# Kernel tuning notes

Measured on AMD Instinct MI355X. Metric: run time of the kernel, lower is better.

Reference implementation:

```python
import jax, jax.numpy as jnp
import numpy as np

B, S, H, NH = 4, 2048, 1024, 16
HS = H // NH  # head size 64


def setup_inputs() -> dict:
    key = jax.random.key(0)
    ks = jax.random.split(key, 12)
    inv = 1.0 / np.sqrt(H)
    d = {
        "query": jax.random.normal(ks[0], (B, S, H), jnp.float32),
        "key": jax.random.normal(ks[1], (B, S, H), jnp.float32),
        "value": jax.random.normal(ks[2], (B, S, H), jnp.float32),
        "causal_mask": jnp.tril(jnp.ones((S, S), dtype=bool)),
        "Wq": jax.random.uniform(ks[3], (H, H), jnp.float32, -inv, inv),
        "bq": jax.random.uniform(ks[4], (H,), jnp.float32, -inv, inv),
        "Wk": jax.random.uniform(ks[5], (H, H), jnp.float32, -inv, inv),
        "bk": jax.random.uniform(ks[6], (H,), jnp.float32, -inv, inv),
        "Wv": jax.random.uniform(ks[7], (H, H), jnp.float32, -inv, inv),
        "bv": jax.random.uniform(ks[8], (H,), jnp.float32, -inv, inv),
        "Wo": jax.random.uniform(ks[9], (H, H), jnp.float32, -inv, inv),
        "bo": jax.random.uniform(ks[10], (H,), jnp.float32, -inv, inv),
    }
    return d


def reference(query, key, value, causal_mask, Wq, bq, Wk, bk, Wv, bv, Wo, bo):
    # Linear projections (torch Linear: x @ W.T + b)
    q = query @ Wq.T + bq
    k = key @ Wk.T + bk
    v = value @ Wv.T + bv
    # [B, NH, S, HS]
    q = q.reshape(B, S, NH, HS).transpose(0, 2, 1, 3)
    k = k.reshape(B, S, NH, HS).transpose(0, 2, 1, 3)
    v = v.reshape(B, S, NH, HS).transpose(0, 2, 1, 3)
    scores = jnp.einsum("bhqd,bhkd->bhqk", q, k) / jnp.sqrt(jnp.float32(HS))
    scores = jnp.where(causal_mask[None, None, :, :], scores, -jnp.inf)
    attn = jax.nn.softmax(scores, axis=-1)
    ctx = jnp.einsum("bhqk,bhkd->bhqd", attn, v)
    ctx = ctx.transpose(0, 2, 1, 3).reshape(B, S, H)
    return ctx @ Wo.T + bo
```

## Files before the change

kernel.cpp:

```cpp
#include <hip/hip_runtime.h>
#include <hip/hip_bf16.h>
#include <math.h>

#define B_  4
#define S_  2048
#define H_  1024
#define NH_ 16
#define HS_ 64

typedef __attribute__((ext_vector_type(8))) short bf16x8;
typedef __attribute__((ext_vector_type(4))) short bf16x4;
typedef __attribute__((ext_vector_type(4))) float f32x4;

#define QSCALE_ (0.125f * 1.44269504f)

__device__ __forceinline__ short f2bf(float f) {
    unsigned u = __builtin_bit_cast(unsigned, f);
    u += 0x7FFFu + ((u >> 16) & 1u);
    return (short)(u >> 16);
}

typedef __attribute__((address_space(3))) void lds_void;
typedef const __attribute__((address_space(1))) void g_void;
__device__ __forceinline__ void gl_lds16(const void* g, void* l) {
    __builtin_amdgcn_global_load_lds((g_void*)g, (lds_void*)l, 16, 0, 0);
}


__global__ __launch_bounds__(256) void cvt_all_k(
    const float* __restrict__ a0, const float* __restrict__ a1,
    const float* __restrict__ a2, const float* __restrict__ w0,
    const float* __restrict__ w1, const float* __restrict__ w2,
    const float* __restrict__ w3,
    short* o0, short* o1, short* o2, short* o3, short* o4, short* o5, short* o6)
{
    const int y = blockIdx.y;
    const float* ins[7]  = {a0, a1, a2, w0, w1, w2, w3};
    short*       outs[7] = {o0, o1, o2, o3, o4, o5, o6};
    const int n8 = (y < 3) ? (int)((size_t)B_ * S_ * H_ / 8) : (int)((size_t)H_ * H_ / 8);
    const int i = blockIdx.x * 256 + threadIdx.x;
    if (i >= n8) return;
    const float4* p = (const float4*)ins[y] + (size_t)i * 2;
    float4 a = p[0], b = p[1];
    bf16x8 o;
    o[0] = f2bf(a.x); o[1] = f2bf(a.y); o[2] = f2bf(a.z); o[3] = f2bf(a.w);
    o[4] = f2bf(b.x); o[5] = f2bf(b.y); o[6] = f2bf(b.z); o[7] = f2bf(b.w);
    *(bf16x8*)(outs[y] + (size_t)i * 8) = o;
}

__device__ __forceinline__ void gemm_core(
    const short* __restrict__ A, const short* __restrict__ W,
    int m0, int n0, short* As, short* Ws, f32x4 acc[4][4])
{
    const int tid  = threadIdx.x;
    const int w    = tid >> 6;
    const int lane = tid & 63;
    const int l15  = lane & 15;
    const int q4   = lane >> 4;
    const int wm   = w >> 1;
    const int wn   = w & 1;
    const int K    = 1024;
    const int swz  = l15 & 7;

    const char* Abase = (const char*)A + (size_t)m0 * K * 2;
    const char* Wbase = (const char*)W + (size_t)n0 * K * 2;

    #pragma unroll
    for (int mi = 0; mi < 4; ++mi)
        #pragma unroll
        for (int ni = 0; ni < 4; ++ni)
            acc[mi][ni] = (f32x4){0.f, 0.f, 0.f, 0.f};

    for (int k0 = 0; k0 < K; k0 += 64) {
        __syncthreads();
        #pragma unroll
        for (int t = 0; t < 4; ++t) {
            const int ob  = t * 4096 + w * 1024;
            const int idx = t * 256 + w * 64 + lane;
            const int row = idx >> 3;
            const int sc  = (idx & 7) ^ (row & 7);
            gl_lds16(Abase + (size_t)row * (K * 2) + k0 * 2 + sc * 16, (char*)As + ob);
            gl_lds16(Wbase + (size_t)row * (K * 2) + k0 * 2 + sc * 16, (char*)Ws + ob);
        }
        __syncthreads();

        #pragma unroll
        for (int kh = 0; kh < 2; ++kh) {
            bf16x8 af[4], bf[4];
            #pragma unroll
            for (int mi = 0; mi < 4; ++mi)
                af[mi] = *(const bf16x8*)(As + (wm * 64 + mi * 16 + l15) * 64
                                             + (((kh * 4 + q4) ^ swz) * 8));
            #pragma unroll
            for (int ni = 0; ni < 4; ++ni)
                bf[ni] = *(const bf16x8*)(Ws + (wn * 64 + ni * 16 + l15) * 64
                                             + (((kh * 4 + q4) ^ swz) * 8));
            #pragma unroll
            for (int mi = 0; mi < 4; ++mi)
                #pragma unroll
                for (int ni = 0; ni < 4; ++ni)
                    acc[mi][ni] = __builtin_amdgcn_mfma_f32_16x16x32_bf16(
                        af[mi], bf[ni], acc[mi][ni], 0, 0, 0);
        }
    }
}

__global__ __launch_bounds__(256) void gemm_proj_k(
    const short* __restrict__ Aq, const short* __restrict__ Wqb,
    const float* __restrict__ bq, short* __restrict__ qb,
    const short* __restrict__ Ak, const short* __restrict__ Wkb,
    const float* __restrict__ bk, short* __restrict__ kb,
    const short* __restrict__ Wvb, const short* __restrict__ Av,
    const float* __restrict__ bv, short* __restrict__ vtb)
{
    __shared__ short As[128 * 64];
    __shared__ short Ws[128 * 64];

    const int z = blockIdx.z;
    const short *A, *W; const float* bias; short* out;
    if (z == 0)      { A = Aq;  W = Wqb; bias = bq; out = qb;  }
    else if (z == 1) { A = Ak;  W = Wkb; bias = bk; out = kb;  }
    else             { A = Wvb; W = Av;  bias = bv; out = vtb; }
    const int m0 = (z == 2 ? blockIdx.y : blockIdx.x) * 128;
    const int n0 = (z == 2 ? blockIdx.x : blockIdx.y) * 128;

    f32x4 acc[4][4];
    gemm_core(A, W, m0, n0, As, Ws, acc);

    const int tid  = threadIdx.x;
    const int w    = tid >> 6;
    const int lane = tid & 63;
    const int l15  = lane & 15;
    const int q4   = lane >> 4;
    const int wm   = w >> 1;
    const int wn   = w & 1;

    #pragma unroll
    for (int mi = 0; mi < 4; ++mi) {
        #pragma unroll
        for (int r = 0; r < 4; ++r) {
            const int m = m0 + wm * 64 + mi * 16 + q4 * 4 + r;
            #pragma unroll
            for (int ni = 0; ni < 4; ++ni) {
                const int n = n0 + wn * 64 + ni * 16 + l15;
                float v = acc[mi][ni][r] + bias[z == 2 ? m : n];
                if (z == 0) v *= QSCALE_;
                if (z != 2) {
                    const int b = m >> 11, s = m & (S_ - 1);
                    const int h = n >> 6,  d = n & (HS_ - 1);
                    out[(((size_t)b * NH_ + h) * S_ + s) * HS_ + d] = f2bf(v);
                } else {
                    const int b = n >> 11, s = n & (S_ - 1);
                    const int h = m >> 6,  d = m & (HS_ - 1);
                    out[(((size_t)b * NH_ + h) * HS_ + d) * S_ + s] = f2bf(v);
                }
            }
        }
    }
}

__global__ __launch_bounds__(256) void gemm_out_k(
    const short* __restrict__ A, const short* __restrict__ W,
    const float* __restrict__ bias, float* __restrict__ Cout)
{
    __shared__ short As[128 * 64];
    __shared__ short Ws[128 * 64];
    const int m0 = blockIdx.x * 128;
    const int n0 = blockIdx.y * 128;

    f32x4 acc[4][4];
    gemm_core(A, W, m0, n0, As, Ws, acc);

    const int tid  = threadIdx.x;
    const int w    = tid >> 6;
    const int lane = tid & 63;
    const int l15  = lane & 15;
    const int q4   = lane >> 4;
    const int wm   = w >> 1;
    const int wn   = w & 1;

    #pragma unroll
    for (int mi = 0; mi < 4; ++mi)
        #pragma unroll
        for (int r = 0; r < 4; ++r) {
            const int m = m0 + wm * 64 + mi * 16 + q4 * 4 + r;
            #pragma unroll
            for (int ni = 0; ni < 4; ++ni) {
                const int n = n0 + wn * 64 + ni * 16 + l15;
                Cout[(size_t)m * H_ + n] = acc[mi][ni][r] + bias[n];
            }
        }
}

#define PPAD_ 72

__global__ __launch_bounds__(256) void attn_mfma(
    const short* __restrict__ Q, const short* __restrict__ K,
    const short* __restrict__ VT, short* __restrict__ O)
{
    __shared__ short Ks[2][64 * 64];
    __shared__ short Vt[2][64 * 64];
    __shared__ short Pl[4][32 * PPAD_];

    const int tid  = threadIdx.x;
    const int w    = tid >> 6;
    const int lane = tid & 63;
    const int l15  = lane & 15;
    const int q4   = lane >> 4;
    const int swz  = l15 & 7;

    const int old = blockIdx.x;
    const int rid = (old & 7) * 128 + (old >> 3);
    const int bh  = rid >> 4;
    const int qt  = 15 - (rid & 15);

    const size_t base = (size_t)bh * S_ * HS_;
    const int b = bh >> 4;
    const int h = bh & 15;

#define STAGE_KV(slot_, kt_)                                                      \
    do {                                                                          \
        _Pragma("unroll")                                                         \
        for (int t = 0; t < 2; ++t) {                                             \
            const int ob  = (slot_) * 8192 + t * 4096 + w * 1024;                 \
            const int idx = t * 256 + w * 64 + lane;        \
            const int r   = idx >> 3;                                             \
            const int sc  = (idx & 7) ^ (r & 7);          \
            gl_lds16(K + base + (size_t)((kt_) * 64 + r) * HS_ + sc * 8,          \
                     (char*)Ks + ob);                                             \
            gl_lds16(VT + base + (size_t)r * S_ + (kt_) * 64 + sc * 8,            \
                     (char*)Vt + ob);                                             \
        }                                                                         \
    } while (0)

    const int ktmax = 2 * qt + 1;

    STAGE_KV(0, 0);

    bf16x8 aQ[2][2];
    #pragma unroll
    for (int mi = 0; mi < 2; ++mi) {
        const int qrow = qt * 128 + w * 32 + mi * 16 + l15;
        #pragma unroll
        for (int kh = 0; kh < 2; ++kh)
            aQ[mi][kh] = *(const bf16x8*)(Q + base + (size_t)qrow * HS_ + kh * 32 + q4 * 8);
    }

    f32x4 accO[2][4];
    float lsum[2];
    #pragma unroll
    for (int mi = 0; mi < 2; ++mi) {
        #pragma unroll
        for (int db = 0; db < 4; ++db) accO[mi][db] = (f32x4){0.f, 0.f, 0.f, 0.f};
        lsum[mi] = 0.f;
    }

    __syncthreads();

    for (int kt = 0; kt <= ktmax; ++kt) {
        const int cur = kt & 1;
        if (kt < ktmax) STAGE_KV(cur ^ 1, kt + 1);

        f32x4 sbT[2][4];
        const short* KsBase = &Ks[cur][0];
        __builtin_amdgcn_s_setprio(1);
        #pragma unroll
        for (int nb = 0; nb < 4; ++nb) {
            const short* krow = KsBase + (nb * 16 + l15) * 64;
            bf16x8 k0 = *(const bf16x8*)(krow + ((q4 ^ swz) * 8));
            bf16x8 k1 = *(const bf16x8*)(krow + (((4 + q4) ^ swz) * 8));
            #pragma unroll
            for (int mi = 0; mi < 2; ++mi) {
                f32x4 a = (f32x4){0.f, 0.f, 0.f, 0.f};
                a = __builtin_amdgcn_mfma_f32_16x16x32_bf16(k0, aQ[mi][0], a, 0, 0, 0);
                a = __builtin_amdgcn_mfma_f32_16x16x32_bf16(k1, aQ[mi][1], a, 0, 0, 0);
                sbT[mi][nb] = a;
            }
        }
        __builtin_amdgcn_s_setprio(0);

        const bool need_mask = (kt >= 2 * qt);
        #pragma unroll
        for (int mi = 0; mi < 2; ++mi) {
            const int qrow = qt * 128 + w * 32 + mi * 16 + l15;
            #pragma unroll
            for (int nb = 0; nb < 4; ++nb) {
                float pr[4];
                #pragma unroll
                for (int r = 0; r < 4; ++r) {
                    float sv = sbT[mi][nb][r];
                    if (need_mask) {
                        const int kj = kt * 64 + nb * 16 + q4 * 4 + r;
                        if (kj > qrow) sv = -INFINITY;
                    }
                    const float p = exp2f(sv);
                    lsum[mi] += p;
                    pr[r] = p;
                }
                unsigned plo, phi;
                asm("v_cvt_pk_bf16_f32 %0, %1, %2" : "=v"(plo) : "v"(pr[0]), "v"(pr[1]));
                asm("v_cvt_pk_bf16_f32 %0, %1, %2" : "=v"(phi) : "v"(pr[2]), "v"(pr[3]));
                uint2 pk; pk.x = plo; pk.y = phi;
                *(uint2*)&Pl[w][(mi * 16 + l15) * PPAD_ + nb * 16 + q4 * 4] = pk;
            }
        }

        bf16x8 aP[2][2];
        #pragma unroll
        for (int mi = 0; mi < 2; ++mi)
            #pragma unroll
            for (int kh = 0; kh < 2; ++kh)
                aP[mi][kh] = *(const bf16x8*)(&Pl[w][(mi * 16 + l15) * PPAD_ + kh * 32 + q4 * 8]);
        const short* VtBase = &Vt[cur][0];
        __builtin_amdgcn_s_setprio(1);
        #pragma unroll
        for (int db = 0; db < 4; ++db) {
            const short* vrow = VtBase + (db * 16 + l15) * 64;
            bf16x8 v0 = *(const bf16x8*)(vrow + ((q4 ^ swz) * 8));
            bf16x8 v1 = *(const bf16x8*)(vrow + (((4 + q4) ^ swz) * 8));
            #pragma unroll
            for (int mi = 0; mi < 2; ++mi) {
                accO[mi][db] = __builtin_amdgcn_mfma_f32_16x16x32_bf16(aP[mi][0], v0, accO[mi][db], 0, 0, 0);
                accO[mi][db] = __builtin_amdgcn_mfma_f32_16x16x32_bf16(aP[mi][1], v1, accO[mi][db], 0, 0, 0);
            }
        }
        __builtin_amdgcn_s_setprio(0);

        __syncthreads();
    }

    #pragma unroll
    for (int mi = 0; mi < 2; ++mi) {
        float ls = lsum[mi];
        ls += __shfl_xor(ls, 16);
        ls += __shfl_xor(ls, 32);
        #pragma unroll
        for (int r = 0; r < 4; ++r) {
            const float inv = 1.f / __shfl(ls, q4 * 4 + r);
            const int orow = qt * 128 + w * 32 + mi * 16 + q4 * 4 + r;
            short* op = O + ((size_t)(b * S_ + orow)) * H_ + h * HS_;
            #pragma unroll
            for (int db = 0; db < 4; ++db)
                op[db * 16 + l15] = f2bf(accO[mi][db][r] * inv);
        }
    }
#undef STAGE_KV
}

extern "C" void kernel_launch(void* const* d_in, const int* in_sizes, int n_in,
                              void* d_out, int out_size, void* d_ws, size_t ws_size,
                              hipStream_t stream)
{
    const float* query = (const float*)d_in[0];
    const float* key   = (const float*)d_in[1];
    const float* value = (const float*)d_in[2];
    const float* Wq = (const float*)d_in[4];
    const float* bq = (const float*)d_in[5];
    const float* Wk = (const float*)d_in[6];
    const float* bk = (const float*)d_in[7];
    const float* Wv = (const float*)d_in[8];
    const float* bv = (const float*)d_in[9];
    const float* Wo = (const float*)d_in[10];
    const float* bo = (const float*)d_in[11];
    float* out = (float*)d_out;

    const size_t EA = (size_t)B_ * S_ * H_;
    const size_t EW = (size_t)H_ * H_;

    short* Aq  = (short*)d_ws;
    short* Ak  = Aq  + EA;
    short* Av  = Ak  + EA;
    short* Wqb = Av  + EA;
    short* Wkb = Wqb + EW;
    short* Wvb = Wkb + EW;
    short* Wob = Wvb + EW;
    short* qb  = Wob + EW;
    short* kb  = qb  + EA;
    short* vtb = kb  + EA;
    short* cb  = vtb + EA;

    const int M = B_ * S_;

    cvt_all_k<<<dim3((int)(EA / 8 / 256), 7), 256, 0, stream>>>(
        query, key, value, Wq, Wk, Wv, Wo,
        Aq, Ak, Av, Wqb, Wkb, Wvb, Wob);

    gemm_proj_k<<<dim3(M / 128, H_ / 128, 3), 256, 0, stream>>>(
        Aq, Wqb, bq, qb, Ak, Wkb, bk, kb, Wvb, Av, bv, vtb);

    attn_mfma<<<dim3(1024), 256, 0, stream>>>(qb, kb, vtb, cb);

    gemm_out_k<<<dim3(M / 128, H_ / 128), 256, 0, stream>>>(cb, Wob, bo, out);
}
```

Baseline: 394.5 us.

## Drop LDS staging in attention; load K/V fragments directly per wave

Rewrites the attention kernel so each wave loads its K and V^T MFMA fragments straight from global memory in 32-key blocks, with no shared-memory double buffering and no __syncthreads. The P tile now stays in registers: the packed bf16 exponentials are fed straight into the PV MFMA instead of going through an LDS round trip. Each wave also runs its own causal trip count (qs), and block-to-XCD mapping uses a new interleaved q-tile order for load balance. This removes LDS traffic and block-wide barriers but relies on L2/L1 for K/V reuse across the four waves, and the V^T fragments come from narrower 8-byte global loads.

```diff
diff --git a/kernel.cpp b/kernel.cpp
--- a/kernel.cpp
+++ b/kernel.cpp
@@ -9,8 +9,9 @@
 #define HS_ 64
 
 typedef __attribute__((ext_vector_type(8))) short bf16x8;
-typedef __attribute__((ext_vector_type(4))) short bf16x4;
+typedef __attribute__((ext_vector_type(4))) short s16x4;
 typedef __attribute__((ext_vector_type(4))) float f32x4;
+typedef __attribute__((ext_vector_type(4))) unsigned u32x4;
 
 #define QSCALE_ (0.125f * 1.44269504f)
 
@@ -25,7 +26,6 @@
 __device__ __forceinline__ void gl_lds16(const void* g, void* l) {
     __builtin_amdgcn_global_load_lds((g_void*)g, (lds_void*)l, 16, 0, 0);
 }
-
 
 __global__ __launch_bounds__(256) void cvt_all_k(
     const float* __restrict__ a0, const float* __restrict__ a1,
@@ -192,55 +192,32 @@
         }
 }
 
-#define PPAD_ 72
-
-__global__ __launch_bounds__(256) void attn_mfma(
+__global__ __launch_bounds__(256, 4) void attn_mfma(
     const short* __restrict__ Q, const short* __restrict__ K,
     const short* __restrict__ VT, short* __restrict__ O)
 {
-    __shared__ short Ks[2][64 * 64];
-    __shared__ short Vt[2][64 * 64];
-    __shared__ short Pl[4][32 * PPAD_];
-
     const int tid  = threadIdx.x;
     const int w    = tid >> 6;
     const int lane = tid & 63;
     const int l15  = lane & 15;
     const int q4   = lane >> 4;
-    const int swz  = l15 & 7;
 
     const int old = blockIdx.x;
-    const int rid = (old & 7) * 128 + (old >> 3);
-    const int bh  = rid >> 4;
-    const int qt  = 15 - (rid & 15);
+    const int pos = old >> 3;
+    const int xcd = old & 7;
+    static const int qtseq[16] = {15,14,13,12, 0,1,2,3, 11,10,9,8, 4,5,6,7};
+    const int bh = xcd * 8 + (pos & 7);
+    const int qt = qtseq[pos >> 3];
+    const int qs = qt * 4 + w;
 
     const size_t base = (size_t)bh * S_ * HS_;
     const int b = bh >> 4;
     const int h = bh & 15;
 
-#define STAGE_KV(slot_, kt_)                                                      \
-    do {                                                                          \
-        _Pragma("unroll")                                                         \
-        for (int t = 0; t < 2; ++t) {                                             \
-            const int ob  = (slot_) * 8192 + t * 4096 + w * 1024;                 \
-            const int idx = t * 256 + w * 64 + lane;        \
-            const int r   = idx >> 3;                                             \
-            const int sc  = (idx & 7) ^ (r & 7);          \
-            gl_lds16(K + base + (size_t)((kt_) * 64 + r) * HS_ + sc * 8,          \
-                     (char*)Ks + ob);                                             \
-            gl_lds16(VT + base + (size_t)r * S_ + (kt_) * 64 + sc * 8,            \
-                     (char*)Vt + ob);                                             \
-        }                                                                         \
-    } while (0)
-
-    const int ktmax = 2 * qt + 1;
-
-    STAGE_KV(0, 0);
-
     bf16x8 aQ[2][2];
     #pragma unroll
     for (int mi = 0; mi < 2; ++mi) {
-        const int qrow = qt * 128 + w * 32 + mi * 16 + l15;
+        const int qrow = qs * 32 + mi * 16 + l15;
         #pragma unroll
         for (int kh = 0; kh < 2; ++kh)
             aQ[mi][kh] = *(const bf16x8*)(Q + base + (size_t)qrow * HS_ + kh * 32 + q4 * 8);
@@ -255,78 +232,82 @@
         lsum[mi] = 0.f;
     }
 
-    __syncthreads();
-
-    for (int kt = 0; kt <= ktmax; ++kt) {
-        const int cur = kt & 1;
-        if (kt < ktmax) STAGE_KV(cur ^ 1, kt + 1);
-
-        f32x4 sbT[2][4];
-        const short* KsBase = &Ks[cur][0];
+    const short* Kb = K  + base;
+    const short* Vb = VT + base;
+
+    for (int kb = 0; kb <= qs; ++kb) {
+        bf16x8 aK[2][2];
+        #pragma unroll
+        for (int nb = 0; nb < 2; ++nb)
+            #pragma unroll
+            for (int kh = 0; kh < 2; ++kh)
+                aK[nb][kh] = *(const bf16x8*)(Kb + (size_t)(kb * 32 + nb * 16 + l15) * HS_
+                                                 + kh * 32 + q4 * 8);
+        bf16x8 vf[4];
+        #pragma unroll
+        for (int db = 0; db < 4; ++db) {
+            const short* vr = Vb + (size_t)(db * 16 + l15) * S_ + kb * 32;
+            s16x4 vlo = *(const s16x4*)(vr + q4 * 4);
+            s16x4 vhi = *(const s16x4*)(vr + 16 + q4 * 4);
+            vf[db] = __builtin_shufflevector(vlo, vhi, 0, 1, 2, 3, 4, 5, 6, 7);
+        }
+
+        f32x4 sT[2][2];
         __builtin_amdgcn_s_setprio(1);
         #pragma unroll
-        for (int nb = 0; nb < 4; ++nb) {
-            const short* krow = KsBase + (nb * 16 + l15) * 64;
-            bf16x8 k0 = *(const bf16x8*)(krow + ((q4 ^ swz) * 8));
-            bf16x8 k1 = *(const bf16x8*)(krow + (((4 + q4) ^ swz) * 8));
-            #pragma unroll
-            for (int mi = 0; mi < 2; ++mi) {
+        for (int mi = 0; mi < 2; ++mi)
+            #pragma unroll
+            for (int nb = 0; nb < 2; ++nb) {
                 f32x4 a = (f32x4){0.f, 0.f, 0.f, 0.f};
-                a = __builtin_amdgcn_mfma_f32_16x16x32_bf16(k0, aQ[mi][0], a, 0, 0, 0);
-                a = __builtin_amdgcn_mfma_f32_16x16x32_bf16(k1, aQ[mi][1], a, 0, 0, 0);
-                sbT[mi][nb] = a;
+                a = __builtin_amdgcn_mfma_f32_16x16x32_bf16(aK[nb][0], aQ[mi][0], a, 0, 0, 0);
+                a = __builtin_amdgcn_mfma_f32_16x16x32_bf16(aK[nb][1], aQ[mi][1], a, 0, 0, 0);
+                sT[mi][nb] = a;
             }
-        }
         __builtin_amdgcn_s_setprio(0);
 
-        const bool need_mask = (kt >= 2 * qt);
+        if (kb == qs) {
+            #pragma unroll
+            for (int mi = 0; mi < 2; ++mi)
+                #pragma unroll
+                for (int nb = 0; nb < 2; ++nb)
+                    #pragma unroll
+                    for (int r = 0; r < 4; ++r) {
+                        const int kloc = nb * 16 + q4 * 4 + r;
+                        const int qloc = mi * 16 + l15;
+                        if (kloc > qloc) sT[mi][nb][r] = -INFINITY;
+                    }
+        }
+
+        bf16x8 aP[2];
         #pragma unroll
         for (int mi = 0; mi < 2; ++mi) {
-            const int qrow = qt * 128 + w * 32 + mi * 16 + l15;
-            #pragma unroll
-            for (int nb = 0; nb < 4; ++nb) {
-                float pr[4];
+            float p[2][4];
+            #pragma unroll
+            for (int nb = 0; nb < 2; ++nb)
                 #pragma unroll
                 for (int r = 0; r < 4; ++r) {
-                    float sv = sbT[mi][nb][r];
-                    if (need_mask) {
-                        const int kj = kt * 64 + nb * 16 + q4 * 4 + r;
-                        if (kj > qrow) sv = -INFINITY;
-                    }
-                    const float p = exp2f(sv);
-                    lsum[mi] += p;
-                    pr[r] = p;
+                    float pv;
+                    asm("v_exp_f32 %0, %1" : "=v"(pv) : "v"(sT[mi][nb][r]));
+                    lsum[mi] += pv;
+                    p[nb][r] = pv;
                 }
-                unsigned plo, phi;
-                asm("v_cvt_pk_bf16_f32 %0, %1, %2" : "=v"(plo) : "v"(pr[0]), "v"(pr[1]));
-                asm("v_cvt_pk_bf16_f32 %0, %1, %2" : "=v"(phi) : "v"(pr[2]), "v"(pr[3]));
-                uint2 pk; pk.x = plo; pk.y = phi;
-                *(uint2*)&Pl[w][(mi * 16 + l15) * PPAD_ + nb * 16 + q4 * 4] = pk;
-            }
-        }
-
-        bf16x8 aP[2][2];
-        #pragma unroll
-        for (int mi = 0; mi < 2; ++mi)
-            #pragma unroll
-            for (int kh = 0; kh < 2; ++kh)
-                aP[mi][kh] = *(const bf16x8*)(&Pl[w][(mi * 16 + l15) * PPAD_ + kh * 32 + q4 * 8]);
-        const short* VtBase = &Vt[cur][0];
+            unsigned w0, w1, w2, w3;
+            asm("v_cvt_pk_bf16_f32 %0, %1, %2" : "=v"(w0) : "v"(p[0][0]), "v"(p[0][1]));
+            asm("v_cvt_pk_bf16_f32 %0, %1, %2" : "=v"(w1) : "v"(p[0][2]), "v"(p[0][3]));
+            asm("v_cvt_pk_bf16_f32 %0, %1, %2" : "=v"(w2) : "v"(p[1][0]), "v"(p[1][1]));
+            asm("v_cvt_pk_bf16_f32 %0, %1, %2" : "=v"(w3) : "v"(p[1][2]), "v"(p[1][3]));
+            u32x4 pw; pw[0] = w0; pw[1] = w1; pw[2] = w2; pw[3] = w3;
+            aP[mi] = __builtin_bit_cast(bf16x8, pw);
+        }
+
         __builtin_amdgcn_s_setprio(1);
         #pragma unroll
-        for (int db = 0; db < 4; ++db) {
-            const short* vrow = VtBase + (db * 16 + l15) * 64;
-            bf16x8 v0 = *(const bf16x8*)(vrow + ((q4 ^ swz) * 8));
-            bf16x8 v1 = *(const bf16x8*)(vrow + (((4 + q4) ^ swz) * 8));
-            #pragma unroll
-            for (int mi = 0; mi < 2; ++mi) {
-                accO[mi][db] = __builtin_amdgcn_mfma_f32_16x16x32_bf16(aP[mi][0], v0, accO[mi][db], 0, 0, 0);
-                accO[mi][db] = __builtin_amdgcn_mfma_f32_16x16x32_bf16(aP[mi][1], v1, accO[mi][db], 0, 0, 0);
-            }
-        }
+        for (int db = 0; db < 4; ++db)
+            #pragma unroll
+            for (int mi = 0; mi < 2; ++mi)
+                accO[mi][db] = __builtin_amdgcn_mfma_f32_16x16x32_bf16(
+                    aP[mi], vf[db], accO[mi][db], 0, 0, 0);
         __builtin_amdgcn_s_setprio(0);
-
-        __syncthreads();
     }
 
     #pragma unroll
@@ -337,14 +318,13 @@
         #pragma unroll
         for (int r = 0; r < 4; ++r) {
             const float inv = 1.f / __shfl(ls, q4 * 4 + r);
-            const int orow = qt * 128 + w * 32 + mi * 16 + q4 * 4 + r;
+            const int orow = qs * 32 + mi * 16 + q4 * 4 + r;
             short* op = O + ((size_t)(b * S_ + orow)) * H_ + h * HS_;
             #pragma unroll
             for (int db = 0; db < 4; ++db)
                 op[db * 16 + l15] = f2bf(accO[mi][db][r] * inv);
         }
     }
-#undef STAGE_KV
 }
 
 extern "C" void kernel_launch(void* const* d_in, const int* in_sizes, int n_in,
```

New measurement: 459.8 us. +16.6%, slower.
